# Kernel tuning notes

Hardware: AMD Instinct MI355X
Metric: run time of the kernel (lower is better)

The kernel has to match this reference:

```python
import jax, jax.numpy as jnp
import numpy as np

IN_FEATURES = 1024
OUT_FEATURES = 512
TAU_U = 20.0
DT = 1.0


def setup_inputs() -> dict:
    key = jax.random.key(0)
    k_x, k_w = jax.random.split(key)
    B, T = 32, 1024
    x = jax.random.normal(k_x, (B, T, IN_FEATURES), dtype=jnp.float32)
    # uniform(-sqrt(1/in), sqrt(1/in)) as in reset_parameters
    bound = float(np.sqrt(1.0 / IN_FEATURES))
    weight = jax.random.uniform(k_w, (OUT_FEATURES, IN_FEATURES), dtype=jnp.float32,
                                minval=-bound, maxval=bound)
    bias = jnp.zeros((OUT_FEATURES,), dtype=jnp.float32)
    # fixed tau trainer: decay = exp(-dt / tau), tau fixed at 20
    decay_u = jnp.full((OUT_FEATURES,), float(np.exp(-DT / TAU_U)), dtype=jnp.float32)
    return {"x": x, "weight": weight, "bias": bias, "decay_u": decay_u}


def reference(x, weight, bias, decay_u):
    # x: [B, T, in] -> current: [B, T, out] (one big GEMM instead of T small ones)
    current = jnp.einsum("bti,oi->bto", x, weight) + bias
    B = x.shape[0]
    u0 = jnp.zeros((B, OUT_FEATURES), dtype=x.dtype)

    drive = (1.0 - decay_u) * current          # [B, T, out]
    drive_t = jnp.swapaxes(drive, 0, 1)        # [T, B, out] for scan

    def step(u_tm1, d_t):
        u_t = decay_u * u_tm1 + d_t
        return u_t, u_t

    _, outs_t = jax.lax.scan(step, u0, drive_t)  # [T, B, out]
    outputs = jnp.swapaxes(outs_t, 0, 1)          # [B, T, out]
    # states: stack([u0, u1, ..., uT], dim=1).unsqueeze(0) -> [1, B, T+1, out]
    states = jnp.concatenate([u0[:, None, :], outputs], axis=1)[None]
    return outputs, states
```

## Files before the change

### kernel.cpp

```cpp
#include <hip/hip_runtime.h>
#include <hip/hip_bf16.h>
#include <stdint.h>

#define BATCH 32
#define SEQT  1024
#define INF   1024
#define OUTF  512
#define MROWS (BATCH * SEQT)

typedef __attribute__((ext_vector_type(8))) short short8;
typedef __attribute__((ext_vector_type(4))) float f32x4;

__device__ __forceinline__ short f2bf(float f) {
    return (short)__builtin_bit_cast(unsigned short, __float2bfloat16(f));
}

__global__ __launch_bounds__(256, 2) void gemm_bf16_kernel(
    const float* __restrict__ X, const float* __restrict__ W,
    const float* __restrict__ bias, __hip_bfloat16* __restrict__ C) {
    __shared__ short lds[2][2][128 * 64];

    const int tid = threadIdx.x;
    const int bid = blockIdx.x;
    const int xcd = bid & 7;
    const int idx = bid >> 3;
    const int mt  = (xcd << 5) + (idx >> 2);
    const int nt  = idx & 3;
    const int m0 = mt << 7;
    const int o0 = nt << 7;

    const int wv   = tid >> 6;
    const int lane = tid & 63;
    const int wr = wv >> 1;
    const int wc = wv & 1;
    const int r0 = lane & 15;
    const int lg = lane >> 4;

    const float* pa[4];
    const float* pb[4];
    int srow[4], skg[4];
#pragma unroll
    for (int it = 0; it < 4; ++it) {
        const int idx2 = (it << 8) + tid;
        srow[it] = idx2 >> 3;
        skg[it]  = idx2 & 7;
        pa[it] = X + (size_t)(m0 + srow[it]) * INF + (skg[it] << 3);
        pb[it] = W + (size_t)(o0 + srow[it]) * INF + (skg[it] << 3);
    }

    f32x4 rA[4][2], rB[4][2];
#pragma unroll
    for (int it = 0; it < 4; ++it) {
        rA[it][0] = *(const f32x4*)(pa[it]);
        rA[it][1] = *(const f32x4*)(pa[it] + 4);
        rB[it][0] = *(const f32x4*)(pb[it]);
        rB[it][1] = *(const f32x4*)(pb[it] + 4);
    }

    f32x4 acc[4][4] = {};

    for (int kt = 0; kt < 16; ++kt) {
        short* la = &lds[kt & 1][0][0];
        short* lb = &lds[kt & 1][1][0];
#pragma unroll
        for (int it = 0; it < 4; ++it) {
            const int row = srow[it];
            const int sw  = (skg[it] ^ (row & 7)) << 3;
            short8 ha, hb;
#pragma unroll
            for (int j = 0; j < 4; ++j) {
                ha[j] = f2bf(rA[it][0][j]); ha[4 + j] = f2bf(rA[it][1][j]);
                hb[j] = f2bf(rB[it][0][j]); hb[4 + j] = f2bf(rB[it][1][j]);
            }
            *(short8*)&la[(row << 6) + sw] = ha;
            *(short8*)&lb[(row << 6) + sw] = hb;
        }
        if (kt < 15) {
            const int kb = (kt + 1) << 6;
#pragma unroll
            for (int it = 0; it < 4; ++it) {
                rA[it][0] = *(const f32x4*)(pa[it] + kb);
                rA[it][1] = *(const f32x4*)(pa[it] + kb + 4);
                rB[it][0] = *(const f32x4*)(pb[it] + kb);
                rB[it][1] = *(const f32x4*)(pb[it] + kb + 4);
            }
        }
        __syncthreads();
#pragma unroll
        for (int kk = 0; kk < 2; ++kk) {
            short8 av[4], bv[4];
#pragma unroll
            for (int mi = 0; mi < 4; ++mi) {
                const int row = (wr << 6) + (mi << 4) + r0;
                const int g   = (kk << 2) + lg;
                av[mi] = *(const short8*)&la[(row << 6) + ((g ^ (row & 7)) << 3)];
            }
#pragma unroll
            for (int ni = 0; ni < 4; ++ni) {
                const int row = (wc << 6) + (ni << 4) + r0;
                const int g   = (kk << 2) + lg;
                bv[ni] = *(const short8*)&lb[(row << 6) + ((g ^ (row & 7)) << 3)];
            }
#pragma unroll
            for (int mi = 0; mi < 4; ++mi)
#pragma unroll
                for (int ni = 0; ni < 4; ++ni)
                    acc[mi][ni] = __builtin_amdgcn_mfma_f32_16x16x32_bf16(
                        av[mi], bv[ni], acc[mi][ni], 0, 0, 0);
        }
    }

    __syncthreads();
    short* cs = &lds[0][0][0];
#pragma unroll
    for (int ni = 0; ni < 4; ++ni) {
        const int col = (wc << 6) + (ni << 4) + r0;
        const float bb = bias[o0 + col];
#pragma unroll
        for (int mi = 0; mi < 4; ++mi) {
            const int rb = (wr << 6) + (mi << 4) + (lg << 2);
#pragma unroll
            for (int j = 0; j < 4; ++j)
                cs[(rb + j) * 136 + col] = f2bf(acc[mi][ni][j] + bb);
        }
    }
    __syncthreads();
    const int r16 = tid >> 4, c16 = tid & 15;
    short* cg = (short*)C;
#pragma unroll
    for (int p = 0; p < 8; ++p) {
        const int row = (p << 4) + r16;
        short8 v = *(const short8*)&cs[row * 136 + (c16 << 3)];
        *(short8*)&cg[(size_t)(m0 + row) * OUTF + o0 + (c16 << 3)] = v;
    }
}

template <bool WRITE_OUT>
__global__ __launch_bounds__(256) void scan_kernel(
    const __hip_bfloat16* __restrict__ cur, float* __restrict__ outp,
    float* __restrict__ states, const float* __restrict__ decay) {
    const int gid = blockIdx.x * 256 + threadIdx.x;
    const int o   = gid & 511;
    const int seg = (gid >> 9) & 7;
    const int b   = gid >> 12;

    const float d   = decay[o];
    const float omd = 1.0f - d;
    const __hip_bfloat16* c = cur + (size_t)b * (SEQT * OUTF) + o;
    float* sp = states + (size_t)b * ((SEQT + 1) * OUTF) + o;

    if (seg == 0) sp[0] = 0.0f;

    float u = 0.0f;
    const int t0 = seg << 7;
    const int tw = (seg == 0) ? 0 : (t0 - 128);
    for (int t = tw; t < t0; t += 8) {
        float r[8];
#pragma unroll
        for (int j = 0; j < 8; ++j) r[j] = __bfloat162float(c[(size_t)(t + j) * OUTF]);
#pragma unroll
        for (int j = 0; j < 8; ++j) u = fmaf(d, u, omd * r[j]);
    }
    float* op = outp + (size_t)b * (SEQT * OUTF) + o;
    for (int t = t0; t < t0 + 128; t += 8) {
        float r[8];
#pragma unroll
        for (int j = 0; j < 8; ++j) r[j] = __bfloat162float(c[(size_t)(t + j) * OUTF]);
        float uu[8];
#pragma unroll
        for (int j = 0; j < 8; ++j) { u = fmaf(d, u, omd * r[j]); uu[j] = u; }
#pragma unroll
        for (int j = 0; j < 8; ++j) sp[(size_t)(t + 1 + j) * OUTF] = uu[j];
        if (WRITE_OUT) {
#pragma unroll
            for (int j = 0; j < 8; ++j) op[(size_t)(t + j) * OUTF] = uu[j];
        }
    }
}

__global__ __launch_bounds__(256) void copy_out_kernel(
    float* __restrict__ outp, const float* __restrict__ states) {
    const size_t total = (size_t)MROWS * OUTF / 4;
    size_t i = (size_t)blockIdx.x * blockDim.x + threadIdx.x;
    const size_t stride = (size_t)gridDim.x * blockDim.x;
    for (; i < total; i += stride) {
        const size_t flat = i * 4;
        const size_t o  = flat & 511;
        const size_t bt = flat >> 9;
        const size_t b  = bt >> 10;
        const size_t t  = bt & 1023;
        *(f32x4*)&outp[flat] =
            *(const f32x4*)&states[(b * (SEQT + 1) + t + 1) * OUTF + o];
    }
}

extern "C" void kernel_launch(void* const* d_in, const int* in_sizes, int n_in,
                              void* d_out, int out_size, void* d_ws, size_t ws_size,
                              hipStream_t stream) {
    const float* x     = (const float*)d_in[0];
    const float* w     = (const float*)d_in[1];
    const float* bias  = (const float*)d_in[2];
    const float* decay = (const float*)d_in[3];

    float* outp   = (float*)d_out;
    float* states = outp + (size_t)MROWS * OUTF;

    const size_t cur_bytes = (size_t)MROWS * OUTF * sizeof(__hip_bfloat16);
    const bool use_ws = (ws_size >= cur_bytes);
    __hip_bfloat16* cur = use_ws ? (__hip_bfloat16*)d_ws : (__hip_bfloat16*)outp;

    gemm_bf16_kernel<<<dim3(1024), dim3(256), 0, stream>>>(x, w, bias, cur);

    if (use_ws) {
        scan_kernel<true><<<dim3(512), dim3(256), 0, stream>>>(cur, outp, states, decay);
    } else {
        scan_kernel<false><<<dim3(512), dim3(256), 0, stream>>>(cur, nullptr, states, decay);
        copy_out_kernel<<<dim3(2048), dim3(256), 0, stream>>>(outp, states);
    }
}
```

Measured before the change: 123.7 us.

## Prefetch X tiles two K-steps ahead with dual register buffers in GEMM

The GEMM main loop now holds two register buffers for the X (A) tiles and loads each one two K-iterations ahead, while W (B) tiles are still loaded one step ahead. The loop is manually unrolled by two through a macro so each phase alternates register buffer and LDS buffer. The aim is to hide more global-load latency for the larger, streamed X operand. The cost is 32 more VGPRs for the extra fp32 prefetch registers, which could hurt the 2-blocks-per-CU occupancy or cause spills under launch_bounds(256,2).

```diff
diff --git a/kernel.cpp b/kernel.cpp
--- a/kernel.cpp
+++ b/kernel.cpp
@@ -48,67 +48,88 @@
         pb[it] = W + (size_t)(o0 + srow[it]) * INF + (skg[it] << 3);
     }
 
-    f32x4 rA[4][2], rB[4][2];
-#pragma unroll
-    for (int it = 0; it < 4; ++it) {
-        rA[it][0] = *(const f32x4*)(pa[it]);
-        rA[it][1] = *(const f32x4*)(pa[it] + 4);
-        rB[it][0] = *(const f32x4*)(pb[it]);
-        rB[it][1] = *(const f32x4*)(pb[it] + 4);
+    f32x4 PA[4][2], QA[4][2], RB[4][2];
+#pragma unroll
+    for (int it = 0; it < 4; ++it) {
+        PA[it][0] = *(const f32x4*)(pa[it]);
+        PA[it][1] = *(const f32x4*)(pa[it] + 4);
+    }
+#pragma unroll
+    for (int it = 0; it < 4; ++it) {
+        RB[it][0] = *(const f32x4*)(pb[it]);
+        RB[it][1] = *(const f32x4*)(pb[it] + 4);
+    }
+#pragma unroll
+    for (int it = 0; it < 4; ++it) {
+        QA[it][0] = *(const f32x4*)(pa[it] + 64);
+        QA[it][1] = *(const f32x4*)(pa[it] + 64 + 4);
     }
 
     f32x4 acc[4][4] = {};
 
-    for (int kt = 0; kt < 16; ++kt) {
-        short* la = &lds[kt & 1][0][0];
-        short* lb = &lds[kt & 1][1][0];
-#pragma unroll
-        for (int it = 0; it < 4; ++it) {
-            const int row = srow[it];
-            const int sw  = (skg[it] ^ (row & 7)) << 3;
-            short8 ha, hb;
-#pragma unroll
-            for (int j = 0; j < 4; ++j) {
-                ha[j] = f2bf(rA[it][0][j]); ha[4 + j] = f2bf(rA[it][1][j]);
-                hb[j] = f2bf(rB[it][0][j]); hb[4 + j] = f2bf(rB[it][1][j]);
-            }
-            *(short8*)&la[(row << 6) + sw] = ha;
-            *(short8*)&lb[(row << 6) + sw] = hb;
-        }
-        if (kt < 15) {
-            const int kb = (kt + 1) << 6;
-#pragma unroll
-            for (int it = 0; it < 4; ++it) {
-                rA[it][0] = *(const f32x4*)(pa[it] + kb);
-                rA[it][1] = *(const f32x4*)(pa[it] + kb + 4);
-                rB[it][0] = *(const f32x4*)(pb[it] + kb);
-                rB[it][1] = *(const f32x4*)(pb[it] + kb + 4);
-            }
-        }
-        __syncthreads();
-#pragma unroll
-        for (int kk = 0; kk < 2; ++kk) {
-            short8 av[4], bv[4];
-#pragma unroll
-            for (int mi = 0; mi < 4; ++mi) {
-                const int row = (wr << 6) + (mi << 4) + r0;
-                const int g   = (kk << 2) + lg;
-                av[mi] = *(const short8*)&la[(row << 6) + ((g ^ (row & 7)) << 3)];
-            }
-#pragma unroll
-            for (int ni = 0; ni < 4; ++ni) {
-                const int row = (wc << 6) + (ni << 4) + r0;
-                const int g   = (kk << 2) + lg;
-                bv[ni] = *(const short8*)&lb[(row << 6) + ((g ^ (row & 7)) << 3)];
-            }
-#pragma unroll
-            for (int mi = 0; mi < 4; ++mi)
-#pragma unroll
-                for (int ni = 0; ni < 4; ++ni)
-                    acc[mi][ni] = __builtin_amdgcn_mfma_f32_16x16x32_bf16(
-                        av[mi], bv[ni], acc[mi][ni], 0, 0, 0);
-        }
-    }
+#define GEMM_PHASE(AREG, BUF, KT)                                            \
+    {                                                                        \
+        short* la = &lds[BUF][0][0];                                         \
+        short* lb = &lds[BUF][1][0];                                         \
+        _Pragma("unroll")                                                    \
+        for (int it = 0; it < 4; ++it) {                                     \
+            const int row = srow[it];                                        \
+            const int sw  = (skg[it] ^ (row & 7)) << 3;                      \
+            short8 ha, hb;                                                   \
+            _Pragma("unroll")                                                \
+            for (int j = 0; j < 4; ++j) {                                    \
+                ha[j] = f2bf(AREG[it][0][j]); ha[4 + j] = f2bf(AREG[it][1][j]); \
+                hb[j] = f2bf(RB[it][0][j]);   hb[4 + j] = f2bf(RB[it][1][j]);   \
+            }                                                                \
+            *(short8*)&la[(row << 6) + sw] = ha;                             \
+            *(short8*)&lb[(row << 6) + sw] = hb;                             \
+        }                                                                    \
+        if ((KT) + 1 < 16) {                \
+            const int kb = ((KT) + 1) << 6;                                  \
+            _Pragma("unroll")                                                \
+            for (int it = 0; it < 4; ++it) {                                 \
+                RB[it][0] = *(const f32x4*)(pb[it] + kb);                    \
+                RB[it][1] = *(const f32x4*)(pb[it] + kb + 4);                \
+            }                                                                \
+        }                                                                    \
+        if ((KT) + 2 < 16) {                   \
+            const int kb = ((KT) + 2) << 6;                                  \
+            _Pragma("unroll")                                                \
+            for (int it = 0; it < 4; ++it) {                                 \
+                AREG[it][0] = *(const f32x4*)(pa[it] + kb);                  \
+                AREG[it][1] = *(const f32x4*)(pa[it] + kb + 4);              \
+            }                                                                \
+        }                                                                    \
+        __syncthreads();                                                     \
+        _Pragma("unroll")                                                    \
+        for (int kk = 0; kk < 2; ++kk) {                                     \
+            short8 av[4], bv[4];                                             \
+            _Pragma("unroll")                                                \
+            for (int mi = 0; mi < 4; ++mi) {                                 \
+                const int row = (wr << 6) + (mi << 4) + r0;                  \
+                const int g   = (kk << 2) + lg;                              \
+                av[mi] = *(const short8*)&la[(row << 6) + ((g ^ (row & 7)) << 3)]; \
+            }                                                                \
+            _Pragma("unroll")                                                \
+            for (int ni = 0; ni < 4; ++ni) {                                 \
+                const int row = (wc << 6) + (ni << 4) + r0;                  \
+                const int g   = (kk << 2) + lg;                              \
+                bv[ni] = *(const short8*)&lb[(row << 6) + ((g ^ (row & 7)) << 3)]; \
+            }                                                                \
+            _Pragma("unroll")                                                \
+            for (int mi = 0; mi < 4; ++mi)                                   \
+                _Pragma("unroll")                                            \
+                for (int ni = 0; ni < 4; ++ni)                               \
+                    acc[mi][ni] = __builtin_amdgcn_mfma_f32_16x16x32_bf16(   \
+                        av[mi], bv[ni], acc[mi][ni], 0, 0, 0);               \
+        }                                                                    \
+    }
+
+    for (int t = 0; t < 16; t += 2) {
+        GEMM_PHASE(PA, 0, t)
+        GEMM_PHASE(QA, 1, t + 1)
+    }
+#undef GEMM_PHASE
 
     __syncthreads();
     short* cs = &lds[0][0][0];
```

Result: faster. 111.2 us (-10.1%).
